# Optimization experiments

Measured on AMD Instinct MI355X. Metric: run time of the kernel, lower is better.

The kernel has to match this reference:

```python
import jax, jax.numpy as jnp
import numpy as np

EMBED_DIM = 1024
LAMBDA_INIT = 0.8
EPS = 1e-5


def setup_inputs() -> dict:
    key = jax.random.key(0)
    ks = jax.random.split(key, 8)
    D = EMBED_DIM
    x = jax.random.normal(ks[0], (4, 2048, D), dtype=jnp.float32)
    # torch Linear weight [out, in]; we store transposed [in, out] for x @ W
    s = 1.0 / np.sqrt(D)
    w_q12 = jax.random.uniform(ks[1], (D, 2 * D), jnp.float32, -s, s)
    w_k12 = jax.random.uniform(ks[2], (D, 2 * D), jnp.float32, -s, s)
    w_v = jax.random.uniform(ks[3], (D, D), jnp.float32, -s, s)
    lambda_q1 = 0.1 * jax.random.normal(ks[4], (D,), jnp.float32)
    lambda_k1 = 0.1 * jax.random.normal(ks[5], (D,), jnp.float32)
    lambda_q2 = 0.1 * jax.random.normal(ks[6], (D,), jnp.float32)
    lambda_k2 = 0.1 * jax.random.normal(ks[7], (D,), jnp.float32)
    return {"x": x, "w_q12": w_q12, "w_k12": w_k12, "w_v": w_v,
            "lambda_q1": lambda_q1, "lambda_k1": lambda_k1,
            "lambda_q2": lambda_q2, "lambda_k2": lambda_k2}


def reference(x, w_q12, w_k12, w_v, lambda_q1, lambda_k1, lambda_q2, lambda_k2):
    D = x.shape[-1]
    scale = D ** (-0.25)
    q12 = jnp.einsum('bsd,de->bse', x, w_q12)
    k12 = jnp.einsum('bsd,de->bse', x, w_k12)
    q1, q2 = jnp.split(q12, 2, axis=-1)
    k1, k2 = jnp.split(k12, 2, axis=-1)
    v = jnp.einsum('bsd,de->bse', x, w_v)
    attn1 = jnp.einsum('bqd,bkd->bqk', q1, k1) * scale
    attn2 = jnp.einsum('bqd,bkd->bqk', q2, k2) * scale
    lam1 = jnp.exp(jnp.sum(lambda_q1 * lambda_k1))
    lam2 = jnp.exp(jnp.sum(lambda_q2 * lambda_k2))
    lam_full = lam1 - lam2 + LAMBDA_INIT
    diff = jax.nn.softmax(attn1, axis=-1) - lam_full * jax.nn.softmax(attn2, axis=-1)
    out = jnp.einsum('bqk,bkd->bqd', diff, v)
    # RMSNorm (no affine), then scale by (1 - lambda_init)
    rms = jnp.sqrt(jnp.mean(out * out, axis=-1, keepdims=True) + EPS)
    return (out / rms) * (1.0 - LAMBDA_INIT)
```

## Files before the change

kernel.cpp:

```cpp
#include <hip/hip_runtime.h>

typedef float f32x4 __attribute__((ext_vector_type(4)));
typedef _Float16 h16x8 __attribute__((ext_vector_type(8)));
typedef _Float16 h16x4 __attribute__((ext_vector_type(4)));

#define GLOAD_LDS16(gp, lp) __builtin_amdgcn_global_load_lds(               \
    (const __attribute__((address_space(1))) void*)(gp),                    \
    (__attribute__((address_space(3))) void*)(lp), 16, 0, 0)

__global__ __launch_bounds__(256) void cast_x(const float* __restrict__ x,
                                              _Float16* __restrict__ xh) {
  long i = (long)blockIdx.x * 256 + threadIdx.x;
  f32x4 a = *(const f32x4*)(x + i * 8);
  f32x4 b = *(const f32x4*)(x + i * 8 + 4);
  h16x8 h;
  h[0] = (_Float16)a[0]; h[1] = (_Float16)a[1];
  h[2] = (_Float16)a[2]; h[3] = (_Float16)a[3];
  h[4] = (_Float16)b[0]; h[5] = (_Float16)b[1];
  h[6] = (_Float16)b[2]; h[7] = (_Float16)b[3];
  *(h16x8*)(xh + i * 8) = h;
}

__global__ __launch_bounds__(256) void tcw(const float* __restrict__ in,
                                           _Float16* __restrict__ out,
                                           int Kd, int Nd, float scale) {
  __shared__ float tile[64][65];
  const int t = threadIdx.x;
  const int k0 = blockIdx.y * 64, n0 = blockIdx.x * 64;
  const int tr = t >> 4, tc = (t & 15) * 4;
#pragma unroll
  for (int i = 0; i < 4; ++i) {
    int r = i * 16 + tr;
    f32x4 a = *(const f32x4*)(in + (long)(k0 + r) * Nd + n0 + tc);
    tile[r][tc + 0] = a[0]; tile[r][tc + 1] = a[1];
    tile[r][tc + 2] = a[2]; tile[r][tc + 3] = a[3];
  }
  __syncthreads();
#pragma unroll
  for (int i = 0; i < 4; ++i) {
    int r = i * 16 + tr;
    h16x4 h;
#pragma unroll
    for (int q = 0; q < 4; ++q) h[q] = (_Float16)(tile[tc + q][r] * scale);
    *(h16x4*)(out + (long)(n0 + r) * Kd + k0 + tc) = h;
  }
}

__global__ __launch_bounds__(256) void trans16(const _Float16* __restrict__ in,
                                               _Float16* __restrict__ out,
                                               int R, int Cd, long ibatch, long obatch) {
  __shared__ _Float16 tile[64][72];
  in += (long)blockIdx.z * ibatch;
  out += (long)blockIdx.z * obatch;
  const int t = threadIdx.x;
  const int r0 = blockIdx.y * 64, c0 = blockIdx.x * 64;
  const int tr = t >> 3, tc8 = (t & 7) * 8;
#pragma unroll
  for (int i = 0; i < 2; ++i) {
    int r = i * 32 + tr;
    h16x8 a = *(const h16x8*)(in + (long)(r0 + r) * Cd + c0 + tc8);
    *(h16x8*)(&tile[r][tc8]) = a;
  }
  __syncthreads();
#pragma unroll
  for (int i = 0; i < 2; ++i) {
    int r = i * 32 + tr;
    h16x8 h;
#pragma unroll
    for (int q = 0; q < 8; ++q) h[q] = tile[tc8 + q][r];
    *(h16x8*)(out + (long)(c0 + r) * R + r0 + tc8) = h;
  }
}

__global__ __launch_bounds__(1024) void lambda_k(const float* __restrict__ lq1,
                                                 const float* __restrict__ lk1,
                                                 const float* __restrict__ lq2,
                                                 const float* __restrict__ lk2,
                                                 float* __restrict__ lam) {
  __shared__ float sh1[16], sh2[16];
  const int t = threadIdx.x;
  float p1 = lq1[t] * lk1[t];
  float p2 = lq2[t] * lk2[t];
#pragma unroll
  for (int off = 1; off < 64; off <<= 1) {
    p1 += __shfl_xor(p1, off);
    p2 += __shfl_xor(p2, off);
  }
  if ((t & 63) == 0) { sh1[t >> 6] = p1; sh2[t >> 6] = p2; }
  __syncthreads();
  if (t == 0) {
    float s1 = 0.f, s2 = 0.f;
    for (int i = 0; i < 16; ++i) { s1 += sh1[i]; s2 += sh2[i]; }
    lam[0] = __expf(s1) - __expf(s2) + 0.8f;
  }
}

template <typename CT>
__global__ __launch_bounds__(256, 2) void gemm_bt(
    const _Float16* __restrict__ A, const _Float16* __restrict__ B,
    CT* __restrict__ C, int K, int lda, int ldb, int ldc,
    long abatch, long bbatch, long cbatch) {
  __shared__ _Float16 As[128 * 64];
  __shared__ _Float16 Bs[128 * 64];
  const int t = threadIdx.x;
  const int lane = t & 63;
  const int wv = t >> 6;
  const int wr = wv >> 1, wc = wv & 1;
  const int lg = lane >> 4, l15 = lane & 15;
  const long z = blockIdx.z;
  const _Float16* Ab = A + z * abatch + (long)(blockIdx.y * 128) * lda;
  const _Float16* Bb = B + z * bbatch + (long)(blockIdx.x * 128) * ldb;
  CT* Cb = C + z * cbatch;

  f32x4 acc[4][4] = {};

  for (int kc = 0; kc < K; kc += 64) {
#pragma unroll
    for (int i = 0; i < 4; ++i) {
      int e = i * 256 + t;
      int r = e >> 3, c8 = e & 7;
      int s8 = c8 ^ (r & 7);
      GLOAD_LDS16(Ab + (long)r * lda + kc + s8 * 8, As + e * 8);
      GLOAD_LDS16(Bb + (long)r * ldb + kc + s8 * 8, Bs + e * 8);
    }
    __syncthreads();
#pragma unroll
    for (int ks = 0; ks < 2; ++ks) {
      h16x8 af[4], bf[4];
#pragma unroll
      for (int m = 0; m < 4; ++m) {
        int r = wr * 64 + m * 16 + l15;
        int kb = (ks * 64 + lg * 16) ^ ((r & 7) << 4);
        af[m] = *(const h16x8*)((const char*)As + r * 128 + kb);
      }
#pragma unroll
      for (int n = 0; n < 4; ++n) {
        int r = wc * 64 + n * 16 + l15;
        int kb = (ks * 64 + lg * 16) ^ ((r & 7) << 4);
        bf[n] = *(const h16x8*)((const char*)Bs + r * 128 + kb);
      }
#pragma unroll
      for (int m = 0; m < 4; ++m)
#pragma unroll
        for (int n = 0; n < 4; ++n)
          acc[m][n] = __builtin_amdgcn_mfma_f32_16x16x32_f16(af[m], bf[n], acc[m][n], 0, 0, 0);
    }
    __syncthreads();
  }

  const int crow0 = blockIdx.y * 128 + wr * 64;
  const int ccol0 = blockIdx.x * 128 + wc * 64;
#pragma unroll
  for (int m = 0; m < 4; ++m)
#pragma unroll
    for (int n = 0; n < 4; ++n)
#pragma unroll
      for (int j = 0; j < 4; ++j) {
        int r = crow0 + m * 16 + lg * 4 + j;
        int c = ccol0 + n * 16 + l15;
        Cb[(long)r * ldc + c] = (CT)acc[m][n][j];
      }
}

__global__ __launch_bounds__(256) void softmax_diff(const float* __restrict__ S1,
                                                    const float* __restrict__ S2,
                                                    _Float16* __restrict__ D,
                                                    const float* __restrict__ lamp) {
  const long row = (long)blockIdx.x * 4 + (threadIdx.x >> 6);
  const int lane = threadIdx.x & 63;
  const float lam = *lamp;
  const float* s1 = S1 + row * 2048;
  const float* s2 = S2 + row * 2048;
  float v1[32], v2[32];
  float m1 = -3e38f, m2 = -3e38f;
#pragma unroll
  for (int j = 0; j < 8; ++j) {
    f32x4 a = *(const f32x4*)(s1 + j * 256 + lane * 4);
    f32x4 b = *(const f32x4*)(s2 + j * 256 + lane * 4);
#pragma unroll
    for (int q = 0; q < 4; ++q) {
      v1[j * 4 + q] = a[q]; v2[j * 4 + q] = b[q];
      m1 = fmaxf(m1, a[q]); m2 = fmaxf(m2, b[q]);
    }
  }
#pragma unroll
  for (int off = 1; off < 64; off <<= 1) {
    m1 = fmaxf(m1, __shfl_xor(m1, off));
    m2 = fmaxf(m2, __shfl_xor(m2, off));
  }
  float l1 = 0.f, l2 = 0.f;
#pragma unroll
  for (int e = 0; e < 32; ++e) {
    v1[e] = __expf(v1[e] - m1); l1 += v1[e];
    v2[e] = __expf(v2[e] - m2); l2 += v2[e];
  }
#pragma unroll
  for (int off = 1; off < 64; off <<= 1) {
    l1 += __shfl_xor(l1, off);
    l2 += __shfl_xor(l2, off);
  }
  const float r1 = 1.f / l1, r2 = lam / l2;
  _Float16* d = D + row * 2048;
#pragma unroll
  for (int j = 0; j < 8; ++j) {
    h16x4 h;
#pragma unroll
    for (int q = 0; q < 4; ++q)
      h[q] = (_Float16)(v1[j * 4 + q] * r1 - v2[j * 4 + q] * r2);
    *(h16x4*)(d + j * 256 + lane * 4) = h;
  }
}

__global__ __launch_bounds__(256) void rmsnorm(const float* __restrict__ O,
                                               float* __restrict__ out) {
  const long row = (long)blockIdx.x * 4 + (threadIdx.x >> 6);
  const int lane = threadIdx.x & 63;
  const float* o = O + row * 1024;
  f32x4 xv[4];
  float ss = 0.f;
#pragma unroll
  for (int j = 0; j < 4; ++j) {
    xv[j] = *(const f32x4*)(o + j * 256 + lane * 4);
#pragma unroll
    for (int q = 0; q < 4; ++q) ss += xv[j][q] * xv[j][q];
  }
#pragma unroll
  for (int off = 1; off < 64; off <<= 1) ss += __shfl_xor(ss, off);
  const float s = 0.2f * rsqrtf(ss * (1.f / 1024.f) + 1e-5f);
  float* po = out + row * 1024;
#pragma unroll
  for (int j = 0; j < 4; ++j) {
    f32x4 r;
#pragma unroll
    for (int q = 0; q < 4; ++q) r[q] = xv[j][q] * s;
    *(f32x4*)(po + j * 256 + lane * 4) = r;
  }
}

extern "C" void kernel_launch(void* const* d_in, const int* in_sizes, int n_in,
                              void* d_out, int out_size, void* d_ws, size_t ws_size,
                              hipStream_t stream) {
  const float* x   = (const float*)d_in[0];
  const float* wq  = (const float*)d_in[1];
  const float* wk  = (const float*)d_in[2];
  const float* wv  = (const float*)d_in[3];
  const float* lq1 = (const float*)d_in[4];
  const float* lk1 = (const float*)d_in[5];
  const float* lq2 = (const float*)d_in[6];
  const float* lk2 = (const float*)d_in[7];
  float* out = (float*)d_out;

  const size_t MB = 1ull << 20;
  char* ws = (char*)d_ws;
  _Float16* xh   = (_Float16*)(ws + 0);
  _Float16* wqT  = (_Float16*)(ws + 16 * MB);
  _Float16* wkT  = (_Float16*)(ws + 20 * MB);
  _Float16* wvT  = (_Float16*)(ws + 24 * MB);
  _Float16* q12  = (_Float16*)(ws + 26 * MB);
  _Float16* k12  = (_Float16*)(ws + 58 * MB);
  _Float16* v    = (_Float16*)(ws + 90 * MB);
  _Float16* vt   = (_Float16*)(ws + 106 * MB);
  float*    S1   = (float*)(ws + 122 * MB);
  float*    S2   = (float*)(ws + 186 * MB);
  _Float16* diff = (_Float16*)(ws + 26 * MB);
  float*    opre = (float*)(ws + 58 * MB);
  float*    lam  = (float*)(ws + 250 * MB);

  const float scale = 0.17677669529663689f;

  cast_x<<<4096, 256, 0, stream>>>(x, xh);
  tcw<<<dim3(32, 16), 256, 0, stream>>>(wq, wqT, 1024, 2048, scale);
  tcw<<<dim3(32, 16), 256, 0, stream>>>(wk, wkT, 1024, 2048, 1.0f);
  tcw<<<dim3(16, 16), 256, 0, stream>>>(wv, wvT, 1024, 1024, 1.0f);
  lambda_k<<<1, 1024, 0, stream>>>(lq1, lk1, lq2, lk2, lam);

  gemm_bt<_Float16><<<dim3(16, 64, 1), 256, 0, stream>>>(xh, wqT, q12, 1024, 1024, 1024, 2048, 0, 0, 0);
  gemm_bt<_Float16><<<dim3(16, 64, 1), 256, 0, stream>>>(xh, wkT, k12, 1024, 1024, 1024, 2048, 0, 0, 0);
  gemm_bt<_Float16><<<dim3(8, 64, 1), 256, 0, stream>>>(xh, wvT, v, 1024, 1024, 1024, 1024, 0, 0, 0);

  trans16<<<dim3(16, 32, 4), 256, 0, stream>>>(v, vt, 2048, 1024, 2048l * 1024, 1024l * 2048);

  gemm_bt<float><<<dim3(16, 16, 4), 256, 0, stream>>>(q12, k12, S1, 1024, 2048, 2048, 2048,
                                                      2048l * 2048, 2048l * 2048, 2048l * 2048);
  gemm_bt<float><<<dim3(16, 16, 4), 256, 0, stream>>>(q12 + 1024, k12 + 1024, S2, 1024, 2048, 2048, 2048,
                                                      2048l * 2048, 2048l * 2048, 2048l * 2048);

  softmax_diff<<<2048, 256, 0, stream>>>(S1, S2, diff, lam);

  gemm_bt<float><<<dim3(8, 16, 4), 256, 0, stream>>>(diff, vt, opre, 2048, 2048, 2048, 1024,
                                                     2048l * 2048, 1024l * 2048, 2048l * 1024);

  rmsnorm<<<2048, 256, 0, stream>>>(opre, out);
}
```

Before: 310.5 us.

## Replace GEMM with 256-tile multi-buffered kernel, fuse QKV projection, store scores in fp16

Replaces the 128x128 GEMM with a 256xN-tile, 512-thread kernel. It uses a 4-deep global-to-LDS pipeline with explicit vmcnt waits, MFMA priority boosting and XCD-aware block remapping. The three projection GEMMs become one launch over a packed QKV weight. Attention scores and the pre-norm output are now written in fp16 instead of fp32, which halves their memory traffic but risks overflow or precision loss in the logits and outputs. The LDS swizzle is dropped, so LDS bank conflicts may rise.

```diff
diff --git a/kernel.cpp b/kernel.cpp
--- a/kernel.cpp
+++ b/kernel.cpp
@@ -95,92 +95,133 @@
   }
 }
 
-template <typename CT>
-__global__ __launch_bounds__(256, 2) void gemm_bt(
+template <int NREP, typename CT>
+__global__ __launch_bounds__(512, 2) void gemm256(
     const _Float16* __restrict__ A, const _Float16* __restrict__ B,
     CT* __restrict__ C, int K, int lda, int ldb, int ldc,
-    long abatch, long bbatch, long cbatch) {
-  __shared__ _Float16 As[128 * 64];
-  __shared__ _Float16 Bs[128 * 64];
+    long abatch, long bbatch, long cbatch, int nbx, int nby) {
+  __shared__ _Float16 As[4][256 * 32];
+  __shared__ _Float16 Bs[4][NREP * 64 * 32];
+
+  const int nwg = gridDim.x;
+  const int orig = blockIdx.x;
+  const int qd = nwg >> 3, rm = nwg & 7;
+  const int xcd = orig & 7, sub = orig >> 3;
+  const int wgid = (xcd < rm ? xcd * (qd + 1) : rm * (qd + 1) + (xcd - rm) * qd) + sub;
+
+  const int bz = wgid / (nbx * nby);
+  const int rem = wgid - bz * nbx * nby;
+  const int by = rem / nbx;
+  const int bx = rem - by * nbx;
+
   const int t = threadIdx.x;
-  const int lane = t & 63;
-  const int wv = t >> 6;
-  const int wr = wv >> 1, wc = wv & 1;
+  const int lane = t & 63, wv = t >> 6;
+  const int wm = wv >> 2, wn = wv & 3;
   const int lg = lane >> 4, l15 = lane & 15;
-  const long z = blockIdx.z;
-  const _Float16* Ab = A + z * abatch + (long)(blockIdx.y * 128) * lda;
-  const _Float16* Bb = B + z * bbatch + (long)(blockIdx.x * 128) * ldb;
-  CT* Cb = C + z * cbatch;
-
-  f32x4 acc[4][4] = {};
-
-  for (int kc = 0; kc < K; kc += 64) {
-#pragma unroll
-    for (int i = 0; i < 4; ++i) {
-      int e = i * 256 + t;
-      int r = e >> 3, c8 = e & 7;
-      int s8 = c8 ^ (r & 7);
-      GLOAD_LDS16(Ab + (long)r * lda + kc + s8 * 8, As + e * 8);
-      GLOAD_LDS16(Bb + (long)r * ldb + kc + s8 * 8, Bs + e * 8);
+
+  const _Float16* Ab = A + (long)bz * abatch + (long)(by * 256) * lda;
+  const _Float16* Bb = B + (long)bz * bbatch + (long)(bx * (NREP * 64)) * ldb;
+
+  auto stage = [&](int Tt, int b) {
+    const int kof = Tt * 32;
+    int c = t;
+    GLOAD_LDS16(Ab + (long)(c >> 2) * lda + kof + (c & 3) * 8, &As[b][c * 8]);
+    c = t + 512;
+    GLOAD_LDS16(Ab + (long)(c >> 2) * lda + kof + (c & 3) * 8, &As[b][c * 8]);
+    c = t;
+    GLOAD_LDS16(Bb + (long)(c >> 2) * ldb + kof + (c & 3) * 8, &Bs[b][c * 8]);
+    if constexpr (NREP == 4) {
+      c = t + 512;
+      GLOAD_LDS16(Bb + (long)(c >> 2) * ldb + kof + (c & 3) * 8, &Bs[b][c * 8]);
     }
-    __syncthreads();
-#pragma unroll
-    for (int ks = 0; ks < 2; ++ks) {
-      h16x8 af[4], bf[4];
-#pragma unroll
-      for (int m = 0; m < 4; ++m) {
-        int r = wr * 64 + m * 16 + l15;
-        int kb = (ks * 64 + lg * 16) ^ ((r & 7) << 4);
-        af[m] = *(const h16x8*)((const char*)As + r * 128 + kb);
-      }
-#pragma unroll
-      for (int n = 0; n < 4; ++n) {
-        int r = wc * 64 + n * 16 + l15;
-        int kb = (ks * 64 + lg * 16) ^ ((r & 7) << 4);
-        bf[n] = *(const h16x8*)((const char*)Bs + r * 128 + kb);
-      }
-#pragma unroll
-      for (int m = 0; m < 4; ++m)
-#pragma unroll
-        for (int n = 0; n < 4; ++n)
-          acc[m][n] = __builtin_amdgcn_mfma_f32_16x16x32_f16(af[m], bf[n], acc[m][n], 0, 0, 0);
+  };
+
+  f32x4 acc[8][NREP] = {};
+  const int NT = K >> 5;
+
+  stage(0, 0);
+  stage(1, 1);
+  stage(2, 2);
+  if constexpr (NREP == 4) asm volatile("s_waitcnt vmcnt(8)" ::: "memory");
+  else                     asm volatile("s_waitcnt vmcnt(6)" ::: "memory");
+  __builtin_amdgcn_s_barrier();
+
+  for (int T = 0; T < NT; ++T) {
+    const int b = T & 3;
+    if (T + 3 < NT) stage(T + 3, (T + 3) & 3);
+
+    const _Float16* Asb = &As[b][0];
+    const _Float16* Bsb = &Bs[b][0];
+    h16x8 af[8], bf[NREP];
+#pragma unroll
+    for (int m = 0; m < 4; ++m)
+      af[m] = *(const h16x8*)(Asb + (wm * 128 + m * 16 + l15) * 32 + lg * 8);
+#pragma unroll
+    for (int n = 0; n < NREP; ++n)
+      bf[n] = *(const h16x8*)(Bsb + (wn * (NREP * 16) + n * 16 + l15) * 32 + lg * 8);
+    __builtin_amdgcn_s_setprio(1);
+#pragma unroll
+    for (int m = 0; m < 4; ++m)
+#pragma unroll
+      for (int n = 0; n < NREP; ++n)
+        acc[m][n] = __builtin_amdgcn_mfma_f32_16x16x32_f16(af[m], bf[n], acc[m][n], 0, 0, 0);
+    __builtin_amdgcn_s_setprio(0);
+#pragma unroll
+    for (int m = 4; m < 8; ++m)
+      af[m] = *(const h16x8*)(Asb + (wm * 128 + m * 16 + l15) * 32 + lg * 8);
+    __builtin_amdgcn_s_setprio(1);
+#pragma unroll
+    for (int m = 4; m < 8; ++m)
+#pragma unroll
+      for (int n = 0; n < NREP; ++n)
+        acc[m][n] = __builtin_amdgcn_mfma_f32_16x16x32_f16(af[m], bf[n], acc[m][n], 0, 0, 0);
+    __builtin_amdgcn_s_setprio(0);
+
+    const int ahead = NT - T - 2;
+    if constexpr (NREP == 4) {
+      if (ahead >= 2)      asm volatile("s_waitcnt vmcnt(8)" ::: "memory");
+      else if (ahead == 1) asm volatile("s_waitcnt vmcnt(4)" ::: "memory");
+      else                 asm volatile("s_waitcnt vmcnt(0)" ::: "memory");
+    } else {
+      if (ahead >= 2)      asm volatile("s_waitcnt vmcnt(6)" ::: "memory");
+      else if (ahead == 1) asm volatile("s_waitcnt vmcnt(3)" ::: "memory");
+      else                 asm volatile("s_waitcnt vmcnt(0)" ::: "memory");
     }
-    __syncthreads();
-  }
-
-  const int crow0 = blockIdx.y * 128 + wr * 64;
-  const int ccol0 = blockIdx.x * 128 + wc * 64;
-#pragma unroll
-  for (int m = 0; m < 4; ++m)
-#pragma unroll
-    for (int n = 0; n < 4; ++n)
-#pragma unroll
-      for (int j = 0; j < 4; ++j) {
-        int r = crow0 + m * 16 + lg * 4 + j;
-        int c = ccol0 + n * 16 + l15;
-        Cb[(long)r * ldc + c] = (CT)acc[m][n][j];
-      }
-}
-
-__global__ __launch_bounds__(256) void softmax_diff(const float* __restrict__ S1,
-                                                    const float* __restrict__ S2,
+    __builtin_amdgcn_s_barrier();
+  }
+
+  CT* Cb = C + (long)bz * cbatch;
+  const int crow0 = by * 256 + wm * 128;
+  const int ccol0 = bx * (NREP * 64) + wn * (NREP * 16);
+#pragma unroll
+  for (int m = 0; m < 8; ++m)
+#pragma unroll
+    for (int n = 0; n < NREP; ++n)
+#pragma unroll
+      for (int j = 0; j < 4; ++j)
+        Cb[(long)(crow0 + m * 16 + lg * 4 + j) * ldc + ccol0 + n * 16 + l15] =
+            (CT)acc[m][n][j];
+}
+
+__global__ __launch_bounds__(256) void softmax_diff(const _Float16* __restrict__ S1,
+                                                    const _Float16* __restrict__ S2,
                                                     _Float16* __restrict__ D,
                                                     const float* __restrict__ lamp) {
   const long row = (long)blockIdx.x * 4 + (threadIdx.x >> 6);
   const int lane = threadIdx.x & 63;
   const float lam = *lamp;
-  const float* s1 = S1 + row * 2048;
-  const float* s2 = S2 + row * 2048;
+  const _Float16* s1 = S1 + row * 2048;
+  const _Float16* s2 = S2 + row * 2048;
   float v1[32], v2[32];
   float m1 = -3e38f, m2 = -3e38f;
 #pragma unroll
-  for (int j = 0; j < 8; ++j) {
-    f32x4 a = *(const f32x4*)(s1 + j * 256 + lane * 4);
-    f32x4 b = *(const f32x4*)(s2 + j * 256 + lane * 4);
-#pragma unroll
-    for (int q = 0; q < 4; ++q) {
-      v1[j * 4 + q] = a[q]; v2[j * 4 + q] = b[q];
-      m1 = fmaxf(m1, a[q]); m2 = fmaxf(m2, b[q]);
+  for (int j = 0; j < 4; ++j) {
+    h16x8 a = ((const h16x8*)s1)[j * 64 + lane];
+    h16x8 b = ((const h16x8*)s2)[j * 64 + lane];
+#pragma unroll
+    for (int q = 0; q < 8; ++q) {
+      v1[j * 8 + q] = (float)a[q]; v2[j * 8 + q] = (float)b[q];
+      m1 = fmaxf(m1, v1[j * 8 + q]); m2 = fmaxf(m2, v2[j * 8 + q]);
     }
   }
 #pragma unroll
@@ -202,39 +243,46 @@
   const float r1 = 1.f / l1, r2 = lam / l2;
   _Float16* d = D + row * 2048;
 #pragma unroll
-  for (int j = 0; j < 8; ++j) {
-    h16x4 h;
-#pragma unroll
-    for (int q = 0; q < 4; ++q)
-      h[q] = (_Float16)(v1[j * 4 + q] * r1 - v2[j * 4 + q] * r2);
-    *(h16x4*)(d + j * 256 + lane * 4) = h;
-  }
-}
-
-__global__ __launch_bounds__(256) void rmsnorm(const float* __restrict__ O,
+  for (int j = 0; j < 4; ++j) {
+    h16x8 h;
+#pragma unroll
+    for (int q = 0; q < 8; ++q)
+      h[q] = (_Float16)(v1[j * 8 + q] * r1 - v2[j * 8 + q] * r2);
+    ((h16x8*)d)[j * 64 + lane] = h;
+  }
+}
+
+__global__ __launch_bounds__(256) void rmsnorm(const _Float16* __restrict__ O,
                                                float* __restrict__ out) {
   const long row = (long)blockIdx.x * 4 + (threadIdx.x >> 6);
   const int lane = threadIdx.x & 63;
-  const float* o = O + row * 1024;
-  f32x4 xv[4];
+  const _Float16* o = O + row * 1024;
+  h16x8 a = ((const h16x8*)o)[lane];
+  h16x8 b = ((const h16x8*)o)[64 + lane];
+  float xa[8], xb[8];
   float ss = 0.f;
 #pragma unroll
-  for (int j = 0; j < 4; ++j) {
-    xv[j] = *(const f32x4*)(o + j * 256 + lane * 4);
-#pragma unroll
-    for (int q = 0; q < 4; ++q) ss += xv[j][q] * xv[j][q];
+  for (int q = 0; q < 8; ++q) {
+    xa[q] = (float)a[q]; xb[q] = (float)b[q];
+    ss += xa[q] * xa[q] + xb[q] * xb[q];
   }
 #pragma unroll
   for (int off = 1; off < 64; off <<= 1) ss += __shfl_xor(ss, off);
   const float s = 0.2f * rsqrtf(ss * (1.f / 1024.f) + 1e-5f);
   float* po = out + row * 1024;
-#pragma unroll
-  for (int j = 0; j < 4; ++j) {
-    f32x4 r;
-#pragma unroll
-    for (int q = 0; q < 4; ++q) r[q] = xv[j][q] * s;
-    *(f32x4*)(po + j * 256 + lane * 4) = r;
-  }
+  f32x4 r;
+#pragma unroll
+  for (int q = 0; q < 4; ++q) r[q] = xa[q] * s;
+  *(f32x4*)(po + lane * 8) = r;
+#pragma unroll
+  for (int q = 0; q < 4; ++q) r[q] = xa[4 + q] * s;
+  *(f32x4*)(po + lane * 8 + 4) = r;
+#pragma unroll
+  for (int q = 0; q < 4; ++q) r[q] = xb[q] * s;
+  *(f32x4*)(po + 512 + lane * 8) = r;
+#pragma unroll
+  for (int q = 0; q < 4; ++q) r[q] = xb[4 + q] * s;
+  *(f32x4*)(po + 512 + lane * 8 + 4) = r;
 }
 
 extern "C" void kernel_launch(void* const* d_in, const int* in_sizes, int n_in,
@@ -253,42 +301,38 @@
   const size_t MB = 1ull << 20;
   char* ws = (char*)d_ws;
   _Float16* xh   = (_Float16*)(ws + 0);
-  _Float16* wqT  = (_Float16*)(ws + 16 * MB);
-  _Float16* wkT  = (_Float16*)(ws + 20 * MB);
-  _Float16* wvT  = (_Float16*)(ws + 24 * MB);
-  _Float16* q12  = (_Float16*)(ws + 26 * MB);
-  _Float16* k12  = (_Float16*)(ws + 58 * MB);
-  _Float16* v    = (_Float16*)(ws + 90 * MB);
+  _Float16* Wp   = (_Float16*)(ws + 16 * MB);
+  _Float16* qkv  = (_Float16*)(ws + 26 * MB);
   _Float16* vt   = (_Float16*)(ws + 106 * MB);
-  float*    S1   = (float*)(ws + 122 * MB);
-  float*    S2   = (float*)(ws + 186 * MB);
+  _Float16* S1   = (_Float16*)(ws + 122 * MB);
+  _Float16* S2   = (_Float16*)(ws + 154 * MB);
+  float*    lam  = (float*)(ws + 186 * MB);
   _Float16* diff = (_Float16*)(ws + 26 * MB);
-  float*    opre = (float*)(ws + 58 * MB);
-  float*    lam  = (float*)(ws + 250 * MB);
+  _Float16* opre = (_Float16*)(ws + 58 * MB);
 
   const float scale = 0.17677669529663689f;
 
   cast_x<<<4096, 256, 0, stream>>>(x, xh);
-  tcw<<<dim3(32, 16), 256, 0, stream>>>(wq, wqT, 1024, 2048, scale);
-  tcw<<<dim3(32, 16), 256, 0, stream>>>(wk, wkT, 1024, 2048, 1.0f);
-  tcw<<<dim3(16, 16), 256, 0, stream>>>(wv, wvT, 1024, 1024, 1.0f);
+  tcw<<<dim3(32, 16), 256, 0, stream>>>(wq, Wp, 1024, 2048, scale);
+  tcw<<<dim3(32, 16), 256, 0, stream>>>(wk, Wp + 2048l * 1024, 1024, 2048, 1.0f);
+  tcw<<<dim3(16, 16), 256, 0, stream>>>(wv, Wp + 4096l * 1024, 1024, 1024, 1.0f);
   lambda_k<<<1, 1024, 0, stream>>>(lq1, lk1, lq2, lk2, lam);
 
-  gemm_bt<_Float16><<<dim3(16, 64, 1), 256, 0, stream>>>(xh, wqT, q12, 1024, 1024, 1024, 2048, 0, 0, 0);
-  gemm_bt<_Float16><<<dim3(16, 64, 1), 256, 0, stream>>>(xh, wkT, k12, 1024, 1024, 1024, 2048, 0, 0, 0);
-  gemm_bt<_Float16><<<dim3(8, 64, 1), 256, 0, stream>>>(xh, wvT, v, 1024, 1024, 1024, 1024, 0, 0, 0);
-
-  trans16<<<dim3(16, 32, 4), 256, 0, stream>>>(v, vt, 2048, 1024, 2048l * 1024, 1024l * 2048);
-
-  gemm_bt<float><<<dim3(16, 16, 4), 256, 0, stream>>>(q12, k12, S1, 1024, 2048, 2048, 2048,
-                                                      2048l * 2048, 2048l * 2048, 2048l * 2048);
-  gemm_bt<float><<<dim3(16, 16, 4), 256, 0, stream>>>(q12 + 1024, k12 + 1024, S2, 1024, 2048, 2048, 2048,
-                                                      2048l * 2048, 2048l * 2048, 2048l * 2048);
+  gemm256<4, _Float16><<<640, 512, 0, stream>>>(xh, Wp, qkv, 1024, 1024, 1024, 5120,
+                                                0, 0, 0, 20, 32);
+
+  trans16<<<dim3(16, 32, 4), 256, 0, stream>>>(qkv + 4096, vt, 2048, 5120,
+                                               2048l * 5120, 1024l * 2048);
+
+  gemm256<4, _Float16><<<256, 512, 0, stream>>>(qkv, qkv + 2048, S1, 1024, 5120, 5120, 2048,
+                                                2048l * 5120, 2048l * 5120, 2048l * 2048, 8, 8);
+  gemm256<4, _Float16><<<256, 512, 0, stream>>>(qkv + 1024, qkv + 3072, S2, 1024, 5120, 5120, 2048,
+                                                2048l * 5120, 2048l * 5120, 2048l * 2048, 8, 8);
 
   softmax_diff<<<2048, 256, 0, stream>>>(S1, S2, diff, lam);
 
-  gemm_bt<float><<<dim3(8, 16, 4), 256, 0, stream>>>(diff, vt, opre, 2048, 2048, 2048, 1024,
-                                                     2048l * 2048, 1024l * 2048, 2048l * 1024);
+  gemm256<2, _Float16><<<256, 512, 0, stream>>>(diff, vt, opre, 2048, 2048, 2048, 1024,
+                                                2048l * 2048, 1024l * 2048, 2048l * 1024, 8, 8);
 
   rmsnorm<<<2048, 256, 0, stream>>>(opre, out);
 }
```

Result: slower. 344.9 us (+11.1%).
